# Kernel optimization log

Hardware: AMD Instinct MI355X
Metric: run time of the kernel (lower is better)

Reference implementation:

```python
import jax, jax.numpy as jnp
import numpy as np

DIM = 256
HEADS = 8
DIM_HEAD = 64
HIDDEN = HEADS * DIM_HEAD
SCALE = DIM_HEAD ** -0.5


def setup_inputs() -> dict:
    key = jax.random.key(0)
    ks = jax.random.split(key, 8)
    std = 0.02
    x = jax.random.normal(ks[0], (2, DIM, 16, 64, 64), dtype=jnp.float32)
    Wq = jax.random.normal(ks[1], (HIDDEN, DIM), dtype=jnp.float32) * std
    Wk = jax.random.normal(ks[2], (HIDDEN, DIM), dtype=jnp.float32) * std
    Wv = jax.random.normal(ks[3], (HIDDEN, DIM), dtype=jnp.float32) * std
    Wg = jax.random.normal(ks[4], (HIDDEN, DIM), dtype=jnp.float32) * std
    bg = jnp.zeros((HIDDEN,), dtype=jnp.float32)
    Wo = jax.random.normal(ks[5], (DIM, HIDDEN), dtype=jnp.float32) * std
    bo = jnp.zeros((DIM,), dtype=jnp.float32)
    return {"x": x, "Wq": Wq, "Wk": Wk, "Wv": Wv, "Wg": Wg, "bg": bg, "Wo": Wo, "bo": bo}


def _proj(x, W):  # 1x1 conv, no bias: (B,C,H,W) @ (O,C) -> (B,O,H,W)
    return jnp.einsum('bchw,oc->bohw', x, W)


def reference(x, Wq, Wk, Wv, Wg, bg, Wo, bo):
    b, c, f, h, w = x.shape
    xf = x.transpose(0, 2, 1, 3, 4).reshape(b * f, c, h, w)  # (bf, c, h, w)
    q = _proj(xf, Wq)
    k = _proj(xf, Wk)
    v = _proj(xf, Wv)
    g = _proj(xf, Wg) + bg[None, :, None, None]
    # softmax over height for q, width for k (pre-reshape, as in torch)
    q = jax.nn.softmax(q, axis=-2)
    k = jax.nn.softmax(k, axis=-1)

    def to_heads(t):  # (bf, H*D, h, w) -> (bf, H, h*w, D)
        return t.reshape(b * f, HEADS, DIM_HEAD, h * w).transpose(0, 1, 3, 2)

    q, k, v, g = map(to_heads, (q, k, v, g))
    q = jax.nn.elu(q) + 1.0
    k = jax.nn.elu(k) + 1.0
    g = jax.nn.sigmoid(g)

    kv = jnp.einsum('bhnd,bhne->bhde', k, v)
    k_sum = k.sum(axis=2)                                   # (bf, H, D)
    z = 1.0 / jnp.maximum(jnp.einsum('bhnd,bhd->bhn', q, k_sum), 1e-6)
    out = jnp.einsum('bhnd,bhde->bhne', q * SCALE, kv)
    out = out * z[..., None] * g                            # (bf, H, n, D)

    out = out.transpose(0, 1, 3, 2).reshape(b * f, HIDDEN, h, w)
    out = jnp.einsum('bchw,oc->bohw', out, Wo) + bo[None, :, None, None]
    return out.reshape(b, f, c, h, w).transpose(0, 2, 1, 3, 4)
```

## Files before the change

kernel.cpp:

```cpp
#include <hip/hip_runtime.h>


typedef unsigned short u16;
typedef unsigned int u32;
typedef __bf16 bf16x8 __attribute__((ext_vector_type(8)));
typedef float f32x4 __attribute__((ext_vector_type(4)));

typedef const __attribute__((address_space(1))) void* gas_t;
typedef __attribute__((address_space(3))) void* las_t;
__device__ __forceinline__ void gll16(const void* g, void* l) {
    __builtin_amdgcn_global_load_lds((gas_t)g, (las_t)l, 16, 0, 0);
}

__device__ inline float bf2f(u16 v) { union { u32 i; float f; } u; u.i = ((u32)v) << 16; return u.f; }
__device__ inline u16 f2bf(float f) {
    union { float f; u32 i; } u; u.f = f;
    u32 r = (u.i + 0x7fffu + ((u.i >> 16) & 1u)) >> 16;
    return (u16)r;
}
__device__ inline void split2(float v, u16& h, u16& l) {
    h = f2bf(v);
    l = f2bf(v - bf2f(h));
}

__global__ void k_cvt_w(const float* __restrict__ Wq, const float* __restrict__ Wk,
                        const float* __restrict__ Wv, const float* __restrict__ Wg,
                        const float* __restrict__ Wo,
                        u16* __restrict__ Wh, u16* __restrict__ Wl,
                        u16* __restrict__ Woh, u16* __restrict__ Wol)
{
    int idx = blockIdx.x * 256 + threadIdx.x;
    if (idx < 524288) {
        int o = idx >> 8, c = idx & 255;
        int which = o >> 9, r = o & 511;
        const float* s = (which == 0) ? Wq : (which == 1) ? Wk : (which == 2) ? Wv : Wg;
        u16 h, l; split2(s[r * 256 + c], h, l);
        Wh[idx] = h; Wl[idx] = l;
    } else {
        int j = idx - 524288;
        if (j < 131072) { u16 h, l; split2(Wo[j], h, l); Woh[j] = h; Wol[j] = l; }
    }
}

__global__ __launch_bounds__(256) void k_cvt_x(const float* __restrict__ x,
                                               u16* __restrict__ xh, u16* __restrict__ xl,
                                               int c0)
{
    __shared__ __align__(16) u16 tileh[64 * 132];
    __shared__ __align__(16) u16 tilel[64 * 132];
    const int t = threadIdx.x;
    const int bfl = blockIdx.y;
    const int bfg = c0 + bfl;
    const int n0 = blockIdx.x * 128;
    const int b_ = bfg >> 4, f_ = bfg & 15;
    for (int s = 0; s < 2; ++s) {
        for (int ch2 = 0; ch2 < 2; ++ch2) {
            __syncthreads();
            for (int p = 0; p < 8; ++p) {
                int cl = p * 16 + (t >> 4);
                int c = ch2 * 128 + cl;
                const float* sp = x + (((size_t)b_ * 256 + c) * 16 + f_) * 4096
                                    + n0 + s * 64 + (t & 15) * 4;
                float4 v = *(const float4*)sp;
                float vv[4] = { v.x, v.y, v.z, v.w };
#pragma unroll
                for (int j = 0; j < 4; ++j) {
                    int nl = (t & 15) * 4 + j;
                    u16 h, l; split2(vv[j], h, l);
                    tileh[nl * 132 + cl] = h;
                    tilel[nl * 132 + cl] = l;
                }
            }
            __syncthreads();
#pragma unroll
            for (int i = 0; i < 4; ++i) {
                int flat = t + i * 256;
                int nn = flat >> 4, cc = flat & 15;
                size_t off = ((size_t)bfl * 4096 + n0 + s * 64 + nn) * 256 + ch2 * 128 + cc * 8;
                *(uint4*)(xh + off) = *(const uint4*)(tileh + nn * 132 + cc * 8);
                *(uint4*)(xl + off) = *(const uint4*)(tilel + nn * 132 + cc * 8);
            }
        }
    }
}

__global__ __launch_bounds__(256) void k_proj(
    const u16* __restrict__ Wh, const u16* __restrict__ Wl,
    const u16* __restrict__ xh, const u16* __restrict__ xl,
    const float* __restrict__ bg,
    u16* __restrict__ kh, u16* __restrict__ kl,
    u16* __restrict__ vh, u16* __restrict__ vl,
    float* __restrict__ qf, float* __restrict__ gf, int pass)
{
    __shared__ __align__(16) char smem[65536];
    u16* Ah = (u16*)smem;
    u16* Al = (u16*)(smem + 16384);
    u16* Bh = (u16*)(smem + 32768);
    u16* Bl = (u16*)(smem + 49152);
    float* Csh = (float*)smem;
    const int t = threadIdx.x;
    const int bfl = blockIdx.z;
    const int by = blockIdx.y;
    const int m0 = (pass == 0) ? (512 + by * 128)
                               : ((by < 4) ? by * 128 : 1536 + (by - 4) * 128);
    const int n0 = blockIdx.x * 128;
    const int lane = t & 63, wv = t >> 6, wm = wv >> 1, wn = wv & 1;
    f32x4 acc[4][4] = {};
    const u16* Aph = Wh + (size_t)m0 * 256;
    const u16* Apl = Wl + (size_t)m0 * 256;
    const u16* Bph = xh + ((size_t)bfl * 4096 + n0) * 256;
    const u16* Bpl = xl + ((size_t)bfl * 4096 + n0) * 256;

    for (int kt = 0; kt < 4; ++kt) {
        const int k0 = kt * 64;
#pragma unroll
        for (int jj = 0; jj < 4; ++jj) {
            int s = wv * 4 + jj;
            int row = s * 8 + (lane >> 3);
            int csrc = (lane & 7) ^ (row & 7);
            size_t go = (size_t)row * 256 + k0 + csrc * 8;
            gll16(Aph + go, Ah + s * 512);
            gll16(Apl + go, Al + s * 512);
            gll16(Bph + go, Bh + s * 512);
            gll16(Bpl + go, Bl + s * 512);
        }
        __syncthreads();
#pragma unroll
        for (int kk = 0; kk < 2; ++kk) {
            bf16x8 afh[4], afl[4], bfh[4], bfl_[4];
#pragma unroll
            for (int i = 0; i < 4; ++i) {
                int ra = wm * 64 + i * 16 + (lane & 15);
                int ca = ((kk * 4 + (lane >> 4)) ^ (ra & 7)) * 8;
                afh[i] = *(const bf16x8*)(Ah + ra * 64 + ca);
                afl[i] = *(const bf16x8*)(Al + ra * 64 + ca);
                int rb = wn * 64 + i * 16 + (lane & 15);
                int cb = ((kk * 4 + (lane >> 4)) ^ (rb & 7)) * 8;
                bfh[i] = *(const bf16x8*)(Bh + rb * 64 + cb);
                bfl_[i] = *(const bf16x8*)(Bl + rb * 64 + cb);
            }
#pragma unroll
            for (int mi = 0; mi < 4; ++mi)
#pragma unroll
                for (int ni = 0; ni < 4; ++ni) {
                    acc[mi][ni] = __builtin_amdgcn_mfma_f32_16x16x32_bf16(afh[mi], bfh[ni], acc[mi][ni], 0, 0, 0);
                    acc[mi][ni] = __builtin_amdgcn_mfma_f32_16x16x32_bf16(afh[mi], bfl_[ni], acc[mi][ni], 0, 0, 0);
                    acc[mi][ni] = __builtin_amdgcn_mfma_f32_16x16x32_bf16(afl[mi], bfh[ni], acc[mi][ni], 0, 0, 0);
                }
        }
        __syncthreads();
    }

    const int sector = m0 >> 9;
    for (int ph = 0; ph < 2; ++ph) {
        if (wn == ph) {
#pragma unroll
            for (int mi = 0; mi < 4; ++mi)
#pragma unroll
                for (int ni = 0; ni < 4; ++ni)
#pragma unroll
                    for (int r = 0; r < 4; ++r) {
                        int gr = wm * 64 + mi * 16 + (lane >> 4) * 4 + r;
                        int gcl = ni * 16 + (lane & 15);
                        Csh[gr * 69 + gcl] = acc[mi][ni][r];
                    }
        }
        __syncthreads();
        if (t < 128) {
            const float* src = Csh + t * 69;
            const int oloc = (m0 & 511) + t;
            const size_t doff = ((size_t)bfl * 512 + oloc) * 4096 + n0 + ph * 64;
            if (sector == 0) {
#pragma unroll
                for (int i = 0; i < 16; ++i) {
                    float4 o = { src[i * 4], src[i * 4 + 1], src[i * 4 + 2], src[i * 4 + 3] };
                    *(float4*)(qf + doff + i * 4) = o;
                }
            } else if (sector == 2) {
#pragma unroll
                for (int i = 0; i < 8; ++i) {
                    union { u16 h[8]; uint4 u; } ph_, pl_;
#pragma unroll
                    for (int j = 0; j < 8; ++j) split2(src[i * 8 + j], ph_.h[j], pl_.h[j]);
                    *(uint4*)(vh + doff + i * 8) = ph_.u;
                    *(uint4*)(vl + doff + i * 8) = pl_.u;
                }
            } else if (sector == 1) {
                float mx = -3.0e38f;
                for (int j = 0; j < 64; ++j) mx = fmaxf(mx, src[j]);
                float sum = 0.f;
                for (int j = 0; j < 64; ++j) sum += expf(src[j] - mx);
                float rs = 1.0f / sum;
#pragma unroll
                for (int i = 0; i < 8; ++i) {
                    union { u16 h[8]; uint4 u; } ph_, pl_;
#pragma unroll
                    for (int j = 0; j < 8; ++j) {
                        float p = expf(src[i * 8 + j] - mx) * rs;
                        split2(p, ph_.h[j], pl_.h[j]);
                    }
                    *(uint4*)(kh + doff + i * 8) = ph_.u;
                    *(uint4*)(kl + doff + i * 8) = pl_.u;
                }
            } else {
                float bgv = bg[oloc];
#pragma unroll
                for (int i = 0; i < 16; ++i) {
                    float4 o;
                    float* po = (float*)&o;
#pragma unroll
                    for (int j = 0; j < 4; ++j)
                        po[j] = 1.0f / (1.0f + expf(-(src[i * 4 + j] + bgv)));
                    *(float4*)(gf + doff + i * 4) = o;
                }
            }
        }
        __syncthreads();
    }
}

__global__ __launch_bounds__(256) void k_smq(float* __restrict__ qf)
{
    __shared__ float img[64 * 65];
    __shared__ float red[256];
    __shared__ float mxv[64];
    __shared__ float smv[64];
    const int t = threadIdx.x;
    float* base = qf + ((size_t)blockIdx.y * 512 + blockIdx.x) * 4096;
#pragma unroll
    for (int i = 0; i < 16; ++i) {
        int n = t + i * 256;
        img[(n >> 6) * 65 + (n & 63)] = base[n];
    }
    __syncthreads();
    const int part = t >> 6, wc = t & 63;
    float mx = -3.0e38f;
    for (int hh = 0; hh < 16; ++hh) mx = fmaxf(mx, img[(part * 16 + hh) * 65 + wc]);
    red[t] = mx;
    __syncthreads();
    if (t < 64) mxv[t] = fmaxf(fmaxf(red[t], red[64 + t]), fmaxf(red[128 + t], red[192 + t]));
    __syncthreads();
    float m = mxv[wc], s = 0.f;
    for (int hh = 0; hh < 16; ++hh) s += expf(img[(part * 16 + hh) * 65 + wc] - m);
    red[t] = s;
    __syncthreads();
    if (t < 64) smv[t] = red[t] + red[64 + t] + red[128 + t] + red[192 + t];
    __syncthreads();
    float rm = mxv[t & 63], rs = 1.0f / smv[t & 63];
#pragma unroll
    for (int i = 0; i < 16; ++i) {
        int n = t + i * 256;
        base[n] = expf(img[(n >> 6) * 65 + (n & 63)] - rm) * rs;
    }
}

__global__ __launch_bounds__(256) void k_kv(
    const u16* __restrict__ kh, const u16* __restrict__ kl,
    const u16* __restrict__ vh, const u16* __restrict__ vl,
    float* __restrict__ kvp, float* __restrict__ vsp, float* __restrict__ ksp)
{
    __shared__ __align__(16) char smem[65536];
    u16* Kh = (u16*)smem;
    u16* Kl = (u16*)(smem + 16384);
    u16* Vh = (u16*)(smem + 32768);
    u16* Vl = (u16*)(smem + 49152);
    float* mrg = (float*)smem;
    const int t = threadIdx.x;
    const int oct = blockIdx.x;
    const int bh = blockIdx.y;
    const int NBH = gridDim.y;
    const int lane = t & 63, wv = t >> 6;
    const size_t hb = (size_t)bh * 64 * 4096;

    f32x4 acc[5][5] = {};
    bf16x8 ones;
#pragma unroll
    for (int j = 0; j < 8; ++j) ones[j] = (lane & 15) == 0 ? (__bf16)1.0f : (__bf16)0.0f;

    for (int cc = 0; cc < 4; ++cc) {
        const int pxc = oct * 512 + cc * 128;
#pragma unroll
        for (int jj = 0; jj < 4; ++jj) {
            int s = wv * 4 + jj;
            int row = s * 4 + (lane >> 4);
            int csrc = (lane & 15) ^ (row & 7);
            size_t go = hb + (size_t)row * 4096 + pxc + csrc * 8;
            gll16(kh + go, Kh + s * 512);
            gll16(kl + go, Kl + s * 512);
            gll16(vh + go, Vh + s * 512);
            gll16(vl + go, Vl + s * 512);
        }
        __syncthreads();
        bf16x8 ah[4], al[4], bh_[4], bl_[4];
#pragma unroll
        for (int i = 0; i < 4; ++i) {
            int ra = i * 16 + (lane & 15);
            int kc = (wv * 4 + (lane >> 4)) ^ (ra & 7);
            int off = ra * 128 + kc * 8;
            ah[i]  = *(const bf16x8*)(Kh + off);
            al[i]  = *(const bf16x8*)(Kl + off);
            bh_[i] = *(const bf16x8*)(Vh + off);
            bl_[i] = *(const bf16x8*)(Vl + off);
        }
#pragma unroll
        for (int di = 0; di < 5; ++di) {
            bf16x8 a = (di < 4) ? ah[di] : ones;
#pragma unroll
            for (int ei = 0; ei < 5; ++ei) {
                bf16x8 b = (ei < 4) ? bh_[ei] : ones;
                acc[di][ei] = __builtin_amdgcn_mfma_f32_16x16x32_bf16(a, b, acc[di][ei], 0, 0, 0);
            }
        }
#pragma unroll
        for (int di = 0; di < 5; ++di) {
            bf16x8 a = (di < 4) ? ah[di] : ones;
#pragma unroll
            for (int ei = 0; ei < 4; ++ei)
                acc[di][ei] = __builtin_amdgcn_mfma_f32_16x16x32_bf16(a, bl_[ei], acc[di][ei], 0, 0, 0);
        }
#pragma unroll
        for (int di = 0; di < 4; ++di)
#pragma unroll
            for (int ei = 0; ei < 5; ++ei) {
                bf16x8 b = (ei < 4) ? bh_[ei] : ones;
                acc[di][ei] = __builtin_amdgcn_mfma_f32_16x16x32_bf16(al[di], b, acc[di][ei], 0, 0, 0);
            }
        __syncthreads();
    }

    float* kvm = mrg;
    float* vsm = mrg + 64 * 68;
    float* ksm = mrg + 64 * 68 + 64;
    for (int i = t; i < 64 * 68 + 128; i += 256) mrg[i] = 0.f;
    __syncthreads();
#pragma unroll
    for (int di = 0; di < 4; ++di)
#pragma unroll
        for (int ei = 0; ei < 4; ++ei)
#pragma unroll
            for (int r = 0; r < 4; ++r) {
                int d = di * 16 + (lane >> 4) * 4 + r;
                int e = ei * 16 + (lane & 15);
                atomicAdd(&kvm[d * 68 + e], acc[di][ei][r]);
            }
    if (lane < 16) {
#pragma unroll
        for (int ei = 0; ei < 4; ++ei) atomicAdd(&vsm[ei * 16 + lane], acc[4][ei][0]);
    }
    if ((lane & 15) == 0) {
#pragma unroll
        for (int di = 0; di < 4; ++di)
#pragma unroll
            for (int r = 0; r < 4; ++r)
                atomicAdd(&ksm[di * 16 + (lane >> 4) * 4 + r], acc[di][4][r]);
    }
    __syncthreads();
    float* op = kvp + ((size_t)oct * NBH + bh) * 4096;
#pragma unroll
    for (int i = 0; i < 16; ++i) {
        int idx = t + i * 256;
        op[idx] = kvm[(idx >> 6) * 68 + (idx & 63)];
    }
    if (t < 64) {
        vsp[((size_t)oct * NBH + bh) * 64 + t] = vsm[t];
        ksp[((size_t)oct * NBH + bh) * 64 + t] = 512.0f + ksm[t];
    }
}

__global__ __launch_bounds__(256) void k_att(
    const float* __restrict__ qf, const float* __restrict__ gf,
    const float* __restrict__ kvp, const float* __restrict__ vsp,
    const float* __restrict__ ksp,
    u16* __restrict__ atth, u16* __restrict__ attl, int NBH)
{
    __shared__ __align__(16) float sh[4352 + 64 + 64 + 64 + 16];
    float* kvl = sh;
    float* vsl = sh + 4352;
    float* ksl = sh + 4416;
    float* csl = sh + 4480;
    float* kstp = sh + 4544;
    const int t = threadIdx.x;
    const int bh = blockIdx.z * 8 + blockIdx.y;
    if (t < 64) {
        float a = 0.f, b = 0.f;
#pragma unroll
        for (int o = 0; o < 8; ++o) {
            a += vsp[((size_t)o * NBH + bh) * 64 + t];
            b += ksp[((size_t)o * NBH + bh) * 64 + t];
        }
        vsl[t] = a; ksl[t] = b;
    }
    __syncthreads();
#pragma unroll
    for (int i = 0; i < 16; ++i) {
        int idx = t + i * 256;
        float s = vsl[idx & 63];
#pragma unroll
        for (int o = 0; o < 8; ++o) s += kvp[((size_t)o * NBH + bh) * 4096 + idx];
        kvl[(idx >> 6) * 68 + (idx & 63)] = s;
    }
    __syncthreads();
    if (t < 64) {
        float s = 0.f;
        for (int d = 0; d < 64; ++d) s += kvl[d * 68 + t];
        csl[t] = s;
    }
    if (t == 64) {
        float s = 0.f;
        for (int d = 0; d < 64; ++d) s += ksl[d];
        kstp[0] = s;
    }
    __syncthreads();
    const int n = blockIdx.x * 256 + t;
    const float* qp = qf + ((size_t)bh * 64) * 4096 + n;
    f32x4 sa[16];
#pragma unroll
    for (int i = 0; i < 16; ++i) sa[i] = *(const f32x4*)&csl[i * 4];
    float sz = kstp[0];
    for (int d = 0; d < 64; ++d) {
        float pq = qp[(size_t)d * 4096];
        sz += pq * ksl[d];
        const f32x4* kr = (const f32x4*)&kvl[d * 68];
#pragma unroll
        for (int i = 0; i < 16; ++i) sa[i] += pq * kr[i];
    }
    float zz = 0.125f / fmaxf(sz, 1e-6f);
    const float* gp = gf + ((size_t)bh * 64) * 4096 + n;
    const size_t ab = (((size_t)(bh >> 3)) * 4096 + n) * 512 + (bh & 7) * 64;
#pragma unroll
    for (int eo = 0; eo < 8; ++eo) {
        union { u16 h[8]; uint4 u; } ph_, pl_;
#pragma unroll
        for (int j = 0; j < 8; ++j) {
            int e = eo * 8 + j;
            float val = sa[e >> 2][e & 3] * zz * gp[(size_t)e * 4096];
            split2(val, ph_.h[j], pl_.h[j]);
        }
        *(uint4*)(atth + ab + eo * 8) = ph_.u;
        *(uint4*)(attl + ab + eo * 8) = pl_.u;
    }
}

__global__ __launch_bounds__(256) void k_out(
    const u16* __restrict__ Woh, const u16* __restrict__ Wol,
    const u16* __restrict__ atth, const u16* __restrict__ attl,
    const float* __restrict__ bo, float* __restrict__ out, int c0)
{
    __shared__ __align__(16) u16 smem[32768];
    u16* Ah = smem;
    u16* Al = smem + 8192;
    u16* Bh = smem + 16384;
    u16* Bl = smem + 24576;
    const int t = threadIdx.x;
    const int bfl = blockIdx.z;
    const int bfg = c0 + bfl;
    const int m0 = blockIdx.y * 128;
    const int n0 = blockIdx.x * 128;
    const int lane = t & 63, wv = t >> 6, wm = wv >> 1, wn = wv & 1;
    f32x4 acc[4][4] = {};
    const u16* Aph = Woh + (size_t)m0 * 512;
    const u16* Apl = Wol + (size_t)m0 * 512;
    const u16* Bph = atth + ((size_t)bfl * 4096 + n0) * 512;
    const u16* Bpl = attl + ((size_t)bfl * 4096 + n0) * 512;
    for (int kt = 0; kt < 8; ++kt) {
        const int k0 = kt * 64;
#pragma unroll
        for (int jj = 0; jj < 4; ++jj) {
            int s = wv * 4 + jj;
            int row = s * 8 + (lane >> 3);
            int csrc = (lane & 7) ^ (row & 7);
            size_t go = (size_t)row * 512 + k0 + csrc * 8;
            gll16(Aph + go, Ah + s * 512);
            gll16(Apl + go, Al + s * 512);
            gll16(Bph + go, Bh + s * 512);
            gll16(Bpl + go, Bl + s * 512);
        }
        __syncthreads();
#pragma unroll
        for (int kk = 0; kk < 2; ++kk) {
            bf16x8 afh[4], afl[4], bfh[4], bfl_[4];
#pragma unroll
            for (int i = 0; i < 4; ++i) {
                int ra = wm * 64 + i * 16 + (lane & 15);
                int ca = ((kk * 4 + (lane >> 4)) ^ (ra & 7)) * 8;
                afh[i] = *(const bf16x8*)(Ah + ra * 64 + ca);
                afl[i] = *(const bf16x8*)(Al + ra * 64 + ca);
                int rb = wn * 64 + i * 16 + (lane & 15);
                int cb = ((kk * 4 + (lane >> 4)) ^ (rb & 7)) * 8;
                bfh[i] = *(const bf16x8*)(Bh + rb * 64 + cb);
                bfl_[i] = *(const bf16x8*)(Bl + rb * 64 + cb);
            }
#pragma unroll
            for (int mi = 0; mi < 4; ++mi)
#pragma unroll
                for (int ni = 0; ni < 4; ++ni) {
                    acc[mi][ni] = __builtin_amdgcn_mfma_f32_16x16x32_bf16(afh[mi], bfh[ni], acc[mi][ni], 0, 0, 0);
                    acc[mi][ni] = __builtin_amdgcn_mfma_f32_16x16x32_bf16(afh[mi], bfl_[ni], acc[mi][ni], 0, 0, 0);
                    acc[mi][ni] = __builtin_amdgcn_mfma_f32_16x16x32_bf16(afl[mi], bfh[ni], acc[mi][ni], 0, 0, 0);
                }
        }
        __syncthreads();
    }
    const int b_ = bfg >> 4, f_ = bfg & 15;
#pragma unroll
    for (int mi = 0; mi < 4; ++mi)
#pragma unroll
        for (int ni = 0; ni < 4; ++ni)
#pragma unroll
            for (int r = 0; r < 4; ++r) {
                int o = m0 + wm * 64 + mi * 16 + (lane >> 4) * 4 + r;
                int nn = n0 + wn * 64 + ni * 16 + (lane & 15);
                out[(((size_t)b_ * 256 + o) * 16 + f_) * 4096 + nn] = acc[mi][ni][r] + bo[o];
            }
}

extern "C" void kernel_launch(void* const* d_in, const int* in_sizes, int n_in,
                              void* d_out, int out_size, void* d_ws, size_t ws_size,
                              hipStream_t stream)
{
    const float* x  = (const float*)d_in[0];
    const float* Wq = (const float*)d_in[1];
    const float* Wk = (const float*)d_in[2];
    const float* Wv = (const float*)d_in[3];
    const float* Wg = (const float*)d_in[4];
    const float* bg = (const float*)d_in[5];
    const float* Wo = (const float*)d_in[6];
    const float* bo = (const float*)d_in[7];
    float* out = (float*)d_out;
    char* ws = (char*)d_ws;

    const size_t PER_BF = 30441472ull;
    const size_t FIXED  = 2621440ull;
    int CH = 32;
    while (CH > 1 && FIXED + (size_t)CH * PER_BF > ws_size) CH >>= 1;
    const int nch = 32 / CH;

    u16* Wh  = (u16*)(ws);
    u16* Wl  = (u16*)(ws + 1048576);
    u16* Woh = (u16*)(ws + 2097152);
    u16* Wol = (u16*)(ws + 2359296);
    char* dyn = ws + FIXED;
    u16*   xh   = (u16*)(dyn);
    u16*   xl   = (u16*)(dyn + (size_t)CH * 2097152);
    u16*   kh   = (u16*)(dyn + (size_t)CH * 4194304);
    u16*   kl   = (u16*)(dyn + (size_t)CH * 8388608);
    u16*   vh   = (u16*)(dyn + (size_t)CH * 12582912);
    u16*   vl   = (u16*)(dyn + (size_t)CH * 16777216);
    u16*   atth = (u16*)(dyn + (size_t)CH * 20971520);
    u16*   attl = (u16*)(dyn + (size_t)CH * 25165824);
    float* kvp  = (float*)(dyn + (size_t)CH * 29360128);
    float* vsp  = (float*)(dyn + (size_t)CH * 30408704);
    float* ksp  = (float*)(dyn + (size_t)CH * 30425088);
    float* qf   = (float*)kh;
    float* gf   = (float*)vh;

    k_cvt_w<<<dim3(2560), dim3(256), 0, stream>>>(Wq, Wk, Wv, Wg, Wo, Wh, Wl, Woh, Wol);

    for (int c = 0; c < nch; ++c) {
        const int c0 = c * CH;
        k_cvt_x<<<dim3(32, CH),    dim3(256), 0, stream>>>(x, xh, xl, c0);
        k_proj <<<dim3(32, 8, CH), dim3(256), 0, stream>>>(Wh, Wl, xh, xl, bg,
                                                           kh, kl, vh, vl, qf, gf, 0);
        k_kv   <<<dim3(8, CH * 8), dim3(256), 0, stream>>>(kh, kl, vh, vl, kvp, vsp, ksp);
        k_proj <<<dim3(32, 8, CH), dim3(256), 0, stream>>>(Wh, Wl, xh, xl, bg,
                                                           kh, kl, vh, vl, qf, gf, 1);
        k_smq  <<<dim3(512, CH),   dim3(256), 0, stream>>>(qf);
        k_att  <<<dim3(16, 8, CH), dim3(256), 0, stream>>>(qf, gf, kvp, vsp, ksp, atth, attl, CH * 8);
        k_out  <<<dim3(32, 2, CH), dim3(256), 0, stream>>>(Woh, Wol, atth, attl, bo, out, c0);
    }
}
```

Before: 1.898 ms.

## Merge projection passes and move attention q·kv product onto MFMA

Combines the two projection launches into a single launch that computes all four projections, with q now written in pixel-major layout. The q softmax kernel is rewritten to read that layout, apply the height softmax per width slice and emit split bf16 hi/lo transposed q. A new merge kernel reduces the kv partials into a transposed bf16 hi/lo kv matrix, with k_sum appended as an extra row and the column sums kept in an aux buffer. The attention kernel then does the q·kv and q·k_sum products with three-pass bf16 MFMA instead of scalar FMAs, and stages its output through LDS for coalesced writes. The cost is a larger workspace, which can force smaller chunks, and the precision of the split-bf16 emulation.

Result: faster. 1.751 ms (-7.8%).

```diff
diff --git a/kernel.cpp b/kernel.cpp
--- a/kernel.cpp
+++ b/kernel.cpp
@@ -88,9 +88,10 @@
     const u16* __restrict__ Wh, const u16* __restrict__ Wl,
     const u16* __restrict__ xh, const u16* __restrict__ xl,
     const float* __restrict__ bg,
+    float* __restrict__ qf,
     u16* __restrict__ kh, u16* __restrict__ kl,
     u16* __restrict__ vh, u16* __restrict__ vl,
-    float* __restrict__ qf, float* __restrict__ gf, int pass)
+    float* __restrict__ gf)
 {
     __shared__ __align__(16) char smem[65536];
     u16* Ah = (u16*)smem;
@@ -101,8 +102,7 @@
     const int t = threadIdx.x;
     const int bfl = blockIdx.z;
     const int by = blockIdx.y;
-    const int m0 = (pass == 0) ? (512 + by * 128)
-                               : ((by < 4) ? by * 128 : 1536 + (by - 4) * 128);
+    const int m0 = (by < 4) ? by * 128 : 512 + (by - 4) * 128;
     const int n0 = blockIdx.x * 128;
     const int lane = t & 63, wv = t >> 6, wm = wv >> 1, wn = wv & 1;
     f32x4 acc[4][4] = {};
@@ -166,17 +166,26 @@
                     }
         }
         __syncthreads();
-        if (t < 128) {
+        if (sector == 0) {
+#pragma unroll
+            for (int rr = 0; rr < 2; ++rr) {
+                int n_loc = rr * 32 + (t >> 3);
+                int oct = t & 7;
+                float* dst = qf + ((size_t)bfl * 4096 + n0 + ph * 64 + n_loc) * 512 + m0;
+#pragma unroll
+                for (int j = 0; j < 4; ++j) {
+                    f32x4 o;
+#pragma unroll
+                    for (int c = 0; c < 4; ++c)
+                        o[c] = Csh[(j * 32 + oct * 4 + c) * 69 + n_loc];
+                    *(f32x4*)(dst + j * 32 + oct * 4) = o;
+                }
+            }
+        } else if (t < 128) {
             const float* src = Csh + t * 69;
             const int oloc = (m0 & 511) + t;
             const size_t doff = ((size_t)bfl * 512 + oloc) * 4096 + n0 + ph * 64;
-            if (sector == 0) {
-#pragma unroll
-                for (int i = 0; i < 16; ++i) {
-                    float4 o = { src[i * 4], src[i * 4 + 1], src[i * 4 + 2], src[i * 4 + 3] };
-                    *(float4*)(qf + doff + i * 4) = o;
-                }
-            } else if (sector == 2) {
+            if (sector == 2) {
 #pragma unroll
                 for (int i = 0; i < 8; ++i) {
                     union { u16 h[8]; uint4 u; } ph_, pl_;
@@ -219,38 +228,51 @@
     }
 }
 
-__global__ __launch_bounds__(256) void k_smq(float* __restrict__ qf)
-{
-    __shared__ float img[64 * 65];
-    __shared__ float red[256];
-    __shared__ float mxv[64];
-    __shared__ float smv[64];
+__global__ __launch_bounds__(256) void k_smq(
+    const float* __restrict__ qf, u16* __restrict__ qTh, u16* __restrict__ qTl)
+{
+    __shared__ float S[4 * 64 * 64];
     const int t = threadIdx.x;
-    float* base = qf + ((size_t)blockIdx.y * 512 + blockIdx.x) * 4096;
-#pragma unroll
-    for (int i = 0; i < 16; ++i) {
-        int n = t + i * 256;
-        img[(n >> 6) * 65 + (n & 63)] = base[n];
-    }
-    __syncthreads();
-    const int part = t >> 6, wc = t & 63;
-    float mx = -3.0e38f;
-    for (int hh = 0; hh < 16; ++hh) mx = fmaxf(mx, img[(part * 16 + hh) * 65 + wc]);
-    red[t] = mx;
-    __syncthreads();
-    if (t < 64) mxv[t] = fmaxf(fmaxf(red[t], red[64 + t]), fmaxf(red[128 + t], red[192 + t]));
-    __syncthreads();
-    float m = mxv[wc], s = 0.f;
-    for (int hh = 0; hh < 16; ++hh) s += expf(img[(part * 16 + hh) * 65 + wc] - m);
-    red[t] = s;
-    __syncthreads();
-    if (t < 64) smv[t] = red[t] + red[64 + t] + red[128 + t] + red[192 + t];
-    __syncthreads();
-    float rm = mxv[t & 63], rs = 1.0f / smv[t & 63];
-#pragma unroll
-    for (int i = 0; i < 16; ++i) {
-        int n = t + i * 256;
-        base[n] = expf(img[(n >> 6) * 65 + (n & 63)] - rm) * rs;
+    const int wblk = blockIdx.x;
+    const int bh = blockIdx.y;
+    const int bfl = bh >> 3, head = bh & 7;
+    const float* qbase = qf + (size_t)bfl * 4096 * 512 + head * 64;
+#pragma unroll
+    for (int r = 0; r < 16; ++r) {
+        int h = r * 4 + (t >> 6);
+        int w = (t >> 4) & 3;
+        int li = t & 15;
+        f32x4 v = *(const f32x4*)(qbase + (size_t)(h * 64 + wblk * 4 + w) * 512 + li * 4);
+        *(f32x4*)(S + ((w * 64 + h) * 64 + li * 4)) = v;
+    }
+    __syncthreads();
+    {
+        int w = t >> 6, d = t & 63;
+        float mx = -3.0e38f;
+        for (int h = 0; h < 64; ++h) mx = fmaxf(mx, S[(w * 64 + h) * 64 + d]);
+        float sum = 0.f;
+        for (int h = 0; h < 64; ++h) {
+            int i = (w * 64 + h) * 64 + d;
+            float e = expf(S[i] - mx);
+            S[i] = e;
+            sum += e;
+        }
+        float rs = 1.0f / sum;
+        for (int h = 0; h < 64; ++h) S[(w * 64 + h) * 64 + d] *= rs;
+    }
+    __syncthreads();
+#pragma unroll
+    for (int r = 0; r < 8; ++r) {
+        int px = r * 32 + (t >> 3);
+        int h = px >> 2, w = px & 3;
+        int oct = t & 7;
+        union { u16 h16[8]; uint4 u; } ph_, pl_;
+#pragma unroll
+        for (int j = 0; j < 8; ++j)
+            split2(S[(w * 64 + h) * 64 + oct * 8 + j], ph_.h16[j], pl_.h16[j]);
+        size_t off = ((size_t)bh * 4096 + h * 64 + wblk * 4 + w) * 64 + oct * 8;
+        *(uint4*)(qTh + off) = ph_.u;
+        *(uint4*)(qTl + off) = pl_.u;
     }
 }
 
@@ -367,20 +389,25 @@
     }
 }
 
-__global__ __launch_bounds__(256) void k_att(
-    const float* __restrict__ qf, const float* __restrict__ gf,
+__global__ __launch_bounds__(256) void k_merge(
     const float* __restrict__ kvp, const float* __restrict__ vsp,
     const float* __restrict__ ksp,
-    u16* __restrict__ atth, u16* __restrict__ attl, int NBH)
-{
-    __shared__ __align__(16) float sh[4352 + 64 + 64 + 64 + 16];
-    float* kvl = sh;
-    float* vsl = sh + 4352;
-    float* ksl = sh + 4416;
-    float* csl = sh + 4480;
-    float* kstp = sh + 4544;
+    u16* __restrict__ kvTh, u16* __restrict__ kvTl,
+    float* __restrict__ aux, int NBH)
+{
+    __shared__ float kv[64 * 68];
+    __shared__ float vsl[64];
+    __shared__ float kslL[64];
     const int t = threadIdx.x;
-    const int bh = blockIdx.z * 8 + blockIdx.y;
+    const int bh = blockIdx.x;
+#pragma unroll
+    for (int i = 0; i < 16; ++i) {
+        int idx = t + i * 256;
+        float s = 0.f;
+#pragma unroll
+        for (int o = 0; o < 8; ++o) s += kvp[((size_t)o * NBH + bh) * 4096 + idx];
+        kv[(idx >> 6) * 68 + (idx & 63)] = s;
+    }
     if (t < 64) {
         float a = 0.f, b = 0.f;
 #pragma unroll
@@ -388,56 +415,150 @@
             a += vsp[((size_t)o * NBH + bh) * 64 + t];
             b += ksp[((size_t)o * NBH + bh) * 64 + t];
         }
-        vsl[t] = a; ksl[t] = b;
-    }
-    __syncthreads();
-#pragma unroll
-    for (int i = 0; i < 16; ++i) {
-        int idx = t + i * 256;
-        float s = vsl[idx & 63];
-#pragma unroll
-        for (int o = 0; o < 8; ++o) s += kvp[((size_t)o * NBH + bh) * 4096 + idx];
-        kvl[(idx >> 6) * 68 + (idx & 63)] = s;
+        vsl[t] = a; kslL[t] = b;
     }
     __syncthreads();
     if (t < 64) {
         float s = 0.f;
-        for (int d = 0; d < 64; ++d) s += kvl[d * 68 + t];
-        csl[t] = s;
+        for (int d = 0; d < 64; ++d) s += kv[d * 68 + t];
+        aux[(size_t)bh * 68 + t] = s + 64.0f * vsl[t];
     }
     if (t == 64) {
         float s = 0.f;
-        for (int d = 0; d < 64; ++d) s += ksl[d];
-        kstp[0] = s;
-    }
-    __syncthreads();
-    const int n = blockIdx.x * 256 + t;
-    const float* qp = qf + ((size_t)bh * 64) * 4096 + n;
-    f32x4 sa[16];
-#pragma unroll
-    for (int i = 0; i < 16; ++i) sa[i] = *(const f32x4*)&csl[i * 4];
-    float sz = kstp[0];
-    for (int d = 0; d < 64; ++d) {
-        float pq = qp[(size_t)d * 4096];
-        sz += pq * ksl[d];
-        const f32x4* kr = (const f32x4*)&kvl[d * 68];
-#pragma unroll
-        for (int i = 0; i < 16; ++i) sa[i] += pq * kr[i];
-    }
-    float zz = 0.125f / fmaxf(sz, 1e-6f);
-    const float* gp = gf + ((size_t)bh * 64) * 4096 + n;
-    const size_t ab = (((size_t)(bh >> 3)) * 4096 + n) * 512 + (bh & 7) * 64;
-#pragma unroll
-    for (int eo = 0; eo < 8; ++eo) {
-        union { u16 h[8]; uint4 u; } ph_, pl_;
-#pragma unroll
-        for (int j = 0; j < 8; ++j) {
-            int e = eo * 8 + j;
-            float val = sa[e >> 2][e & 3] * zz * gp[(size_t)e * 4096];
-            split2(val, ph_.h[j], pl_.h[j]);
-        }
-        *(uint4*)(atth + ab + eo * 8) = ph_.u;
-        *(uint4*)(attl + ab + eo * 8) = pl_.u;
+        for (int d = 0; d < 64; ++d) s += kslL[d];
+        aux[(size_t)bh * 68 + 64] = s;
+    }
+    __syncthreads();
+    {
+        int m = t >> 2, kq = t & 3;
+        union { u16 h[16]; uint4 u[2]; } hh, ll;
+        float vm = vsl[m];
+#pragma unroll
+        for (int i = 0; i < 16; ++i) {
+            int k = kq * 16 + i;
+            split2(kv[k * 68 + m] + vm, hh.h[i], ll.h[i]);
+        }
+        size_t off = (size_t)bh * 5120 + (size_t)m * 64 + kq * 16;
+        *(uint4*)(kvTh + off) = hh.u[0];
+        *(uint4*)(kvTh + off + 8) = hh.u[1];
+        *(uint4*)(kvTl + off) = ll.u[0];
+        *(uint4*)(kvTl + off + 8) = ll.u[1];
+    }
+    if (t < 64) {
+        int m2 = 64 + (t >> 2), kq = t & 3;
+        union { u16 h[16]; uint4 u[2]; } hh, ll;
+#pragma unroll
+        for (int i = 0; i < 16; ++i) {
+            float v = (m2 == 64) ? kslL[kq * 16 + i] : 0.f;
+            split2(v, hh.h[i], ll.h[i]);
+        }
+        size_t off = (size_t)bh * 5120 + (size_t)m2 * 64 + kq * 16;
+        *(uint4*)(kvTh + off) = hh.u[0];
+        *(uint4*)(kvTh + off + 8) = hh.u[1];
+        *(uint4*)(kvTl + off) = ll.u[0];
+        *(uint4*)(kvTl + off + 8) = ll.u[1];
+    }
+}
+
+__global__ __launch_bounds__(256) void k_att(
+    const u16* __restrict__ qTh_g, const u16* __restrict__ qTl_g,
+    const float* __restrict__ gf,
+    const u16* __restrict__ kvTh_g, const u16* __restrict__ kvTl_g,
+    const float* __restrict__ aux,
+    u16* __restrict__ atth, u16* __restrict__ attl)
+{
+    __shared__ __align__(16) char smem[71680];
+    u16* qh_s = (u16*)smem;
+    u16* ql_s = (u16*)(smem + 32768);
+    u16* ah_s = (u16*)smem;
+    u16* al_s = (u16*)(smem + 34816);
+    float* szl = (float*)(smem + 69632);
+    float* cslL = (float*)(smem + 70656);
+    const int t = threadIdx.x;
+    const int lane = t & 63, wv = t >> 6;
+    const int row = lane & 15, oct = lane >> 4;
+    const int bh = blockIdx.y;
+    const int bfl = bh >> 3, head = bh & 7;
+    const int n0 = blockIdx.x * 256;
+
+    const u16* qhb = qTh_g + ((size_t)bh * 4096 + n0) * 64;
+    const u16* qlb = qTl_g + ((size_t)bh * 4096 + n0) * 64;
+#pragma unroll
+    for (int r = 0; r < 8; ++r) {
+        int chunk = r * 256 + t;
+        int n = chunk >> 3, c = chunk & 7;
+        size_t src = (size_t)n * 64 + (size_t)((c ^ (n & 7)) * 8);
+        gll16(qhb + src, qh_s + r * 2048 + wv * 512);
+        gll16(qlb + src, ql_s + r * 2048 + wv * 512);
+    }
+    if (t < 65) cslL[t] = aux[(size_t)bh * 68 + t];
+    __syncthreads();
+
+    f32x4 acc[5][4] = {};
+    const u16* Ahg = kvTh_g + (size_t)bh * 5120;
+    const u16* Alg = kvTl_g + (size_t)bh * 5120;
+#pragma unroll
+    for (int pass = 0; pass < 3; ++pass) {
+        const u16* Ap = (pass == 2) ? Alg : Ahg;
+        const u16* Bp = (pass == 1) ? ql_s : qh_s;
+#pragma unroll
+        for (int ks = 0; ks < 2; ++ks) {
+            bf16x8 af[5], bq[4];
+#pragma unroll
+            for (int mi = 0; mi < 5; ++mi)
+                af[mi] = *(const bf16x8*)(Ap + (size_t)(mi * 16 + row) * 64 + ks * 32 + oct * 8);
+#pragma unroll
+            for (int ni = 0; ni < 4; ++ni) {
+                int n_loc = wv * 64 + ni * 16 + row;
+                int chs = ((ks * 4 + oct) ^ (n_loc & 7)) * 8;
+                bq[ni] = *(const bf16x8*)(Bp + n_loc * 64 + chs);
+            }
+#pragma unroll
+            for (int mi = 0; mi < 5; ++mi)
+#pragma unroll
+                for (int ni = 0; ni < 4; ++ni)
+                    acc[mi][ni] = __builtin_amdgcn_mfma_f32_16x16x32_bf16(af[mi], bq[ni], acc[mi][ni], 0, 0, 0);
+        }
+    }
+    if (oct == 0) {
+#pragma unroll
+        for (int ni = 0; ni < 4; ++ni)
+            szl[wv * 64 + ni * 16 + row] = acc[4][ni][0];
+    }
+    __syncthreads();
+
+    const float kstp = cslL[64];
+#pragma unroll
+    for (int ni = 0; ni < 4; ++ni) {
+        int n_loc = wv * 64 + ni * 16 + row;
+        int n_g = n0 + n_loc;
+        float zz = 0.125f / fmaxf(szl[n_loc] + kstp, 1e-6f);
+#pragma unroll
+        for (int mi = 0; mi < 4; ++mi) {
+            int e0 = mi * 16 + oct * 4;
+            u16 hh[4], ll2[4];
+#pragma unroll
+            for (int r2 = 0; r2 < 4; ++r2) {
+                int e = e0 + r2;
+                float g = gf[((size_t)bfl * 512 + head * 64 + e) * 4096 + n_g];
+                float val = (acc[mi][ni][r2] + cslL[e]) * zz * g;
+                split2(val, hh[r2], ll2[r2]);
+            }
+            *(u32*)(ah_s + n_loc * 68 + e0)     = (u32)hh[0] | ((u32)hh[1] << 16);
+            *(u32*)(ah_s + n_loc * 68 + e0 + 2) = (u32)hh[2] | ((u32)hh[3] << 16);
+            *(u32*)(al_s + n_loc * 68 + e0)     = (u32)ll2[0] | ((u32)ll2[1] << 16);
+            *(u32*)(al_s + n_loc * 68 + e0 + 2) = (u32)ll2[2] | ((u32)ll2[3] << 16);
+        }
+    }
+    __syncthreads();
+    u16* gh = atth + ((size_t)bfl * 4096 + n0) * 512 + head * 64;
+    u16* gl = attl + ((size_t)bfl * 4096 + n0) * 512 + head * 64;
+#pragma unroll
+    for (int r = 0; r < 16; ++r) {
+        int n_loc = r * 16 + (t >> 4);
+        int u2 = t & 15;
+        *(uint2*)(gh + (size_t)n_loc * 512 + u2 * 4) = *(const uint2*)(ah_s + n_loc * 68 + u2 * 4);
+        *(uint2*)(gl + (size_t)n_loc * 512 + u2 * 4) = *(const uint2*)(al_s + n_loc * 68 + u2 * 4);
     }
 }
 
@@ -529,7 +650,7 @@
     float* out = (float*)d_out;
     char* ws = (char*)d_ws;
 
-    const size_t PER_BF = 30441472ull;
+    const size_t PER_BF = 47386624ull;
     const size_t FIXED  = 2621440ull;
     int CH = 32;
     while (CH > 1 && FIXED + (size_t)CH * PER_BF > ws_size) CH >>= 1;
@@ -546,26 +667,30 @@
     u16*   kl   = (u16*)(dyn + (size_t)CH * 8388608);
     u16*   vh   = (u16*)(dyn + (size_t)CH * 12582912);
     u16*   vl   = (u16*)(dyn + (size_t)CH * 16777216);
-    u16*   atth = (u16*)(dyn + (size_t)CH * 20971520);
-    u16*   attl = (u16*)(dyn + (size_t)CH * 25165824);
-    float* kvp  = (float*)(dyn + (size_t)CH * 29360128);
-    float* vsp  = (float*)(dyn + (size_t)CH * 30408704);
-    float* ksp  = (float*)(dyn + (size_t)CH * 30425088);
-    float* qf   = (float*)kh;
-    float* gf   = (float*)vh;
+    float* qf   = (float*)(dyn + (size_t)CH * 20971520);
+    float* gf   = (float*)(dyn + (size_t)CH * 29360128);
+    u16*   qTh  = (u16*)(dyn + (size_t)CH * 37748736);
+    u16*   qTl  = (u16*)(dyn + (size_t)CH * 41943040);
+    float* kvp  = (float*)(dyn + (size_t)CH * 46137344);
+    float* vsp  = (float*)(dyn + (size_t)CH * 47185920);
+    float* ksp  = (float*)(dyn + (size_t)CH * 47202304);
+    u16*   kvTh = (u16*)(dyn + (size_t)CH * 47218688);
+    u16*   kvTl = (u16*)(dyn + (size_t)CH * 47300608);
+    float* aux  = (float*)(dyn + (size_t)CH * 47382528);
+    u16*   atth = kh;
+    u16*   attl = kl;
 
     k_cvt_w<<<dim3(2560), dim3(256), 0, stream>>>(Wq, Wk, Wv, Wg, Wo, Wh, Wl, Woh, Wol);
 
     for (int c = 0; c < nch; ++c) {
         const int c0 = c * CH;
-        k_cvt_x<<<dim3(32, CH),    dim3(256), 0, stream>>>(x, xh, xl, c0);
-        k_proj <<<dim3(32, 8, CH), dim3(256), 0, stream>>>(Wh, Wl, xh, xl, bg,
-                                                           kh, kl, vh, vl, qf, gf, 0);
-        k_kv   <<<dim3(8, CH * 8), dim3(256), 0, stream>>>(kh, kl, vh, vl, kvp, vsp, ksp);
-        k_proj <<<dim3(32, 8, CH), dim3(256), 0, stream>>>(Wh, Wl, xh, xl, bg,
-                                                           kh, kl, vh, vl, qf, gf, 1);
-        k_smq  <<<dim3(512, CH),   dim3(256), 0, stream>>>(qf);
-        k_att  <<<dim3(16, 8, CH), dim3(256), 0, stream>>>(qf, gf, kvp, vsp, ksp, atth, attl, CH * 8);
-        k_out  <<<dim3(32, 2, CH), dim3(256), 0, stream>>>(Woh, Wol, atth, attl, bo, out, c0);
-    }
-}
+        k_cvt_x<<<dim3(32, CH),     dim3(256), 0, stream>>>(x, xh, xl, c0);
+        k_proj <<<dim3(32, 16, CH), dim3(256), 0, stream>>>(Wh, Wl, xh, xl, bg,
+                                                            qf, kh, kl, vh, vl, gf);
+        k_kv   <<<dim3(8, CH * 8),  dim3(256), 0, stream>>>(kh, kl, vh, vl, kvp, vsp, ksp);
+        k_merge<<<dim3(CH * 8),     dim3(256), 0, stream>>>(kvp, vsp, ksp, kvTh, kvTl, aux, CH * 8);
+        k_smq  <<<dim3(16, CH * 8), dim3(256), 0, stream>>>(qf, qTh, qTl);
+        k_att  <<<dim3(16, CH * 8), dim3(256), 0, stream>>>(qTh, qTl, gf, kvTh, kvTl, aux, atth, attl);
+        k_out  <<<dim3(32, 2, CH),  dim3(256), 0, stream>>>(Woh, Wol, atth, attl, bo, out, c0);
+    }
+}
```
